# Kernel tuning notes

Measured on AMD Instinct MI355X. Metric: run time of the kernel, lower is better.

The kernel has to match this reference:

```python
import jax, jax.numpy as jnp
import numpy as np

# SectorAttention (PARTNER): dim=256, resolution=(4,4096), H_sp=4, W_sp=1, H=4, heads=8
B, Hq, Hres, Wres, C, NH = 4, 4, 4, 4096, 256, 8
H_SP, W_SP = 4, 1
HD = C // NH
SCALE = HD ** -0.5


def _forward(s, x, s_pos, x_pos, Wq, bq, Wk, bk, Wv, bv, Wo, bo,
             pw1, pb1, bn_g, bn_b, bn_m, bn_v, pw2, pb2,
             ln_g, ln_b, mw1, mb1, mw2, mb2):
    Bb, Lq, Cc = s.shape
    W = Wres
    nW = Bb * (W // W_SP)
    # ---- dynamic relative-position bias (per-window small conv net) ----
    xp = x_pos.reshape(Bb, Hq // H_SP, H_SP, W // W_SP, W_SP, 2)
    xp = jnp.transpose(xp, (0, 1, 3, 5, 2, 4)).reshape(-1, 2, H_SP * W_SP)   # (nW,2,4)
    sp = jnp.transpose(s_pos, (0, 2, 3, 1)).reshape(-1, 2, Hq * W_SP)        # (nW,2,4)
    rel = sp[:, :, :, None] - xp[:, :, None, :]                              # (nW,2,4,4)
    rel = rel.reshape(nW, 2, -1)                                             # (nW,2,16)
    h = jnp.einsum('oc,bcl->bol', pw1, rel) + pb1[None, :, None]             # Conv1d k=1
    h = (h - bn_m[None, :, None]) * jax.lax.rsqrt(bn_v[None, :, None] + 1e-5) \
        * bn_g[None, :, None] + bn_b[None, :, None]                          # BatchNorm1d (eval)
    h = jax.nn.relu(h)
    h = jnp.einsum('oc,bcl->bol', pw2, h) + pb2[None, :, None]               # Conv1d k=1 -> heads
    rel_bias = h.reshape(-1, NH, Hq, H_SP)                                   # (nW,NH,4,4) since W_SP==1
    # ---- projections + window partitioning ----
    q = s @ Wq.T + bq
    q = q.reshape(Bb, Cc, Hq, W)                          # faithful torch .view reinterpretation
    q = q.reshape(Bb, NH, HD, Hq, W // W_SP, W_SP)
    q = jnp.transpose(q, (0, 4, 1, 3, 5, 2)).reshape(-1, NH, Hq * W_SP, HD)

    def im2cswin(t):
        t = jnp.transpose(t, (0, 2, 1)).reshape(Bb, Cc, Hres, W)
        t = t.reshape(Bb, Cc, Hres // H_SP, H_SP, W // W_SP, W_SP)
        t = jnp.transpose(t, (0, 2, 4, 3, 5, 1)).reshape(-1, H_SP * W_SP, Cc)
        return jnp.transpose(t.reshape(-1, H_SP * W_SP, NH, HD), (0, 2, 1, 3))

    k = im2cswin(x @ Wk.T + bk)
    v = im2cswin(x @ Wv.T + bv)
    # ---- windowed attention with dynamic bias ----
    attn = jnp.einsum('wnqd,wnkd->wnqk', q * SCALE, k) + rel_bias
    attn = jax.nn.softmax(attn, axis=-1)
    o = jnp.einsum('wnqk,wnkd->wnqd', attn, v)            # (nW,NH,4,HD)
    o = jnp.transpose(o, (0, 2, 1, 3)).reshape(-1, Hq * W_SP, Cc)
    # windows2img(o, H_sp=Hq, W_sp=W_SP, H=Hq, W=W)
    o = o.reshape(Bb, Hq // Hq, W // W_SP, Hq, W_SP, Cc)
    o = jnp.transpose(o, (0, 1, 3, 2, 4, 5)).reshape(Bb, Hq * W, Cc)
    o = o @ Wo.T + bo
    s1 = s + o
    # ---- LayerNorm + MLP (residual) ----
    mu = jnp.mean(s1, axis=-1, keepdims=True)
    var = jnp.mean((s1 - mu) ** 2, axis=-1, keepdims=True)
    n = (s1 - mu) * jax.lax.rsqrt(var + 1e-5) * ln_g + ln_b
    h2 = jax.nn.gelu(n @ mw1.T + mb1, approximate=False)
    return s1 + h2 @ mw2.T + mb2


def setup_inputs() -> dict:
    key = jax.random.key(0)
    ks = jax.random.split(key, 12)
    rn = lambda k, sh, sc=1.0: jax.random.normal(k, sh, dtype=jnp.float32) * sc
    H4 = 4 * C
    return {
        's': rn(ks[0], (B, Hq * Wres, C)),
        'x': rn(ks[1], (B, Hres * Wres, C)),
        's_pos': rn(ks[2], (B, 2, Wres // W_SP, Hq * W_SP)),
        'x_pos': rn(ks[3], (B, Hres * Wres, 2)),
        'Wq': rn(ks[4], (C, C), 0.02), 'bq': jnp.zeros((C,), jnp.float32),
        'Wk': rn(ks[5], (C, C), 0.02), 'bk': jnp.zeros((C,), jnp.float32),
        'Wv': rn(ks[6], (C, C), 0.02), 'bv': jnp.zeros((C,), jnp.float32),
        'Wo': rn(ks[7], (C, C), 0.02), 'bo': jnp.zeros((C,), jnp.float32),
        'pw1': rn(ks[8], (16, 2), 0.2), 'pb1': jnp.zeros((16,), jnp.float32),
        'bn_g': jnp.ones((16,), jnp.float32), 'bn_b': jnp.zeros((16,), jnp.float32),
        'bn_m': jnp.zeros((16,), jnp.float32), 'bn_v': jnp.ones((16,), jnp.float32),
        'pw2': rn(ks[9], (NH, 16), 0.2), 'pb2': jnp.zeros((NH,), jnp.float32),
        'ln_g': jnp.ones((C,), jnp.float32), 'ln_b': jnp.zeros((C,), jnp.float32),
        'mw1': rn(ks[10], (H4, C), 0.02), 'mb1': jnp.zeros((H4,), jnp.float32),
        'mw2': rn(ks[11], (C, H4), 0.02), 'mb2': jnp.zeros((C,), jnp.float32),
    }


def reference(s, x, s_pos, x_pos, Wq, bq, Wk, bk, Wv, bv, Wo, bo,
              pw1, pb1, bn_g, bn_b, bn_m, bn_v, pw2, pb2,
              ln_g, ln_b, mw1, mb1, mw2, mb2):
    return _forward(s, x, s_pos, x_pos, Wq, bq, Wk, bk, Wv, bv, Wo, bo,
                    pw1, pb1, bn_g, bn_b, bn_m, bn_v, pw2, pb2,
                    ln_g, ln_b, mw1, mb1, mw2, mb2)
```

## Files before the change

### kernel.cpp

```cpp
#include <hip/hip_runtime.h>
#include <hip/hip_bf16.h>
#include <math.h>

typedef __hip_bfloat16 BF;
typedef __bf16 bf16x8 __attribute__((ext_vector_type(8)));
typedef float f32x4 __attribute__((ext_vector_type(4)));

struct alignas(8) BF4 { BF v[4]; };

static __device__ __forceinline__ float b2f(BF x) { return __bfloat162float(x); }
static __device__ __forceinline__ BF f2b(float x) { return __float2bfloat16(x); }

static __device__ __forceinline__ void gld_lds16(const void* g, void* l) {
  __builtin_amdgcn_global_load_lds(
      (const __attribute__((address_space(1))) unsigned int*)g,
      (__attribute__((address_space(3))) unsigned int*)l, 16, 0, 0);
}

__global__ void __launch_bounds__(256) cvt_kernel(
    const float* __restrict__ in, BF* __restrict__ out, int n4) {
  for (int i = blockIdx.x * 256 + threadIdx.x; i < n4; i += gridDim.x * 256) {
    float4 v = ((const float4*)in)[i];
    BF4 o;
    o.v[0] = f2b(v.x); o.v[1] = f2b(v.y); o.v[2] = f2b(v.z); o.v[3] = f2b(v.w);
    ((BF4*)out)[i] = o;
  }
}

__global__ void __launch_bounds__(256) cvt_kv_kernel(
    const float* __restrict__ Wk, const float* __restrict__ Wv,
    const float* __restrict__ bk, const float* __restrict__ bv,
    BF* __restrict__ Wkv, float* __restrict__ bkv) {
  int u = blockIdx.x * 256 + threadIdx.x;
  int r = u >> 5, c8 = u & 31;
  const float* src = ((r & 1) ? Wv : Wk) + (size_t)(r >> 1) * 256 + c8 * 8;
  float4 a = ((const float4*)src)[0];
  float4 b = ((const float4*)src)[1];
  BF tmp[8];
  tmp[0] = f2b(a.x); tmp[1] = f2b(a.y); tmp[2] = f2b(a.z); tmp[3] = f2b(a.w);
  tmp[4] = f2b(b.x); tmp[5] = f2b(b.y); tmp[6] = f2b(b.z); tmp[7] = f2b(b.w);
  *(bf16x8*)(Wkv + (size_t)r * 256 + c8 * 8) = *(bf16x8*)tmp;
  if (u < 512) bkv[u] = ((u & 1) ? bv : bk)[u >> 1];
}

__global__ void __launch_bounds__(256) bias_kernel(
    const float* __restrict__ s_pos, const float* __restrict__ x_pos,
    const float* __restrict__ pw1, const float* __restrict__ pb1,
    const float* __restrict__ bn_g, const float* __restrict__ bn_b,
    const float* __restrict__ bn_m, const float* __restrict__ bn_v,
    const float* __restrict__ pw2, const float* __restrict__ pb2,
    float* __restrict__ out) {
  int gid = blockIdx.x * 256 + threadIdx.x;
  int w = gid >> 4, l = gid & 15;
  int b = w >> 12, wi = w & 4095;
  int i = l >> 2, j = l & 3;
  int e0 = i, e1 = 4 + i;
  float sp0 = s_pos[(((size_t)b * 2 + (e0 & 1)) * 4096 + wi) * 4 + (e0 >> 1)];
  float sp1 = s_pos[(((size_t)b * 2 + (e1 & 1)) * 4096 + wi) * 4 + (e1 >> 1)];
  float xp0 = x_pos[((size_t)b * 16384 + j * 4096 + wi) * 2 + 0];
  float xp1 = x_pos[((size_t)b * 16384 + j * 4096 + wi) * 2 + 1];
  float r0 = sp0 - xp0, r1 = sp1 - xp1;
  float acc[8];
#pragma unroll
  for (int p = 0; p < 8; ++p) acc[p] = pb2[p];
#pragma unroll
  for (int o = 0; o < 16; ++o) {
    float t = pw1[o * 2 + 0] * r0 + pw1[o * 2 + 1] * r1 + pb1[o];
    float sc = bn_g[o] / sqrtf(bn_v[o] + 1e-5f);
    t = (t - bn_m[o]) * sc + bn_b[o];
    t = fmaxf(t, 0.0f);
#pragma unroll
    for (int p = 0; p < 8; ++p) acc[p] += pw2[p * 16 + o] * t;
  }
#pragma unroll
  for (int p = 0; p < 8; ++p) out[(size_t)w * 128 + p * 16 + l] = acc[p];
}

enum { EPI_NONE = 0, EPI_RES = 1, EPI_GELU = 2 };

template <int EPI, typename AT, typename RT, typename CT>
__global__ void __launch_bounds__(256, 2) gemm_tn(
    const AT* __restrict__ A, const BF* __restrict__ Bw,
    const float* __restrict__ bias, const RT* __restrict__ Res,
    CT* __restrict__ C, int M, int N, int K) {
  constexpr bool F32A = __is_same(AT, float);
  alignas(16) __shared__ BF As[2][8][128][8];
  alignas(16) __shared__ BF Bs[2][8][128][8];
  const int ntiles = N >> 7;
  const int cpx = gridDim.x >> 3;
  const int bid = blockIdx.x;
  const int swz = (bid & 7) * cpx + (bid >> 3);
  const int mt = swz / ntiles, nt = swz % ntiles;
  const int row0 = mt << 7, col0 = nt << 7;
  const int t = threadIdx.x;
  const int wave = t >> 6, lane = t & 63;
  const int wr = wave >> 1, wc = wave & 1;
  const int sm = t & 127;
  const int skc = t >> 7;
  f32x4 acc[4][4] = {};
  const int NT = K >> 6;
  float4 ar[4][2];

  auto stageB = [&](int kt, int dbuf) {
#pragma unroll
    for (int i = 0; i < 4; ++i) {
      const int kc = i * 2 + skc;
      gld_lds16(Bw + (size_t)(col0 + sm) * K + kt * 64 + kc * 8,
                &Bs[dbuf][0][0][0] + (size_t)(i * 256 + wave * 64) * 8);
    }
  };
  auto loadA = [&](int kt) {
    if constexpr (F32A) {
#pragma unroll
      for (int i = 0; i < 4; ++i) {
        const int kc = i * 2 + skc;
        const float* src = A + (size_t)(row0 + sm) * K + kt * 64 + kc * 8;
        ar[i][0] = ((const float4*)src)[0];
        ar[i][1] = ((const float4*)src)[1];
      }
    }
  };
  auto writeA = [&](int dbuf) {
    if constexpr (F32A) {
#pragma unroll
      for (int i = 0; i < 4; ++i) {
        const int kc = i * 2 + skc;
        BF tmp[8];
        tmp[0] = f2b(ar[i][0].x); tmp[1] = f2b(ar[i][0].y);
        tmp[2] = f2b(ar[i][0].z); tmp[3] = f2b(ar[i][0].w);
        tmp[4] = f2b(ar[i][1].x); tmp[5] = f2b(ar[i][1].y);
        tmp[6] = f2b(ar[i][1].z); tmp[7] = f2b(ar[i][1].w);
        *(bf16x8*)(&As[dbuf][kc][sm][0]) = *(bf16x8*)tmp;
      }
    }
  };
  auto stageA_bf = [&](int kt, int dbuf) {
    if constexpr (!F32A) {
#pragma unroll
      for (int i = 0; i < 4; ++i) {
        const int kc = i * 2 + skc;
        gld_lds16((const BF*)A + (size_t)(row0 + sm) * K + kt * 64 + kc * 8,
                  &As[dbuf][0][0][0] + (size_t)(i * 256 + wave * 64) * 8);
      }
    }
  };
  auto compute = [&](int dbuf) {
#pragma unroll
    for (int kk = 0; kk < 2; ++kk) {
      const int chunk = kk * 4 + (lane >> 4);
      const int rl = lane & 15;
      bf16x8 af[4], bfr[4];
#pragma unroll
      for (int mi = 0; mi < 4; ++mi)
        af[mi] = *(const bf16x8*)(&As[dbuf][chunk][wr * 64 + mi * 16 + rl][0]);
#pragma unroll
      for (int ni = 0; ni < 4; ++ni)
        bfr[ni] = *(const bf16x8*)(&Bs[dbuf][chunk][wc * 64 + ni * 16 + rl][0]);
#pragma unroll
      for (int mi = 0; mi < 4; ++mi)
#pragma unroll
        for (int ni = 0; ni < 4; ++ni)
          acc[mi][ni] = __builtin_amdgcn_mfma_f32_16x16x32_bf16(
              af[mi], bfr[ni], acc[mi][ni], 0, 0, 0);
    }
  };

  loadA(0); stageA_bf(0, 0); stageB(0, 0); writeA(0);
  __syncthreads();
  int cur = 0;
  for (int kt = 0; kt < NT; ++kt) {
    const bool more = (kt + 1 < NT);
    if (more) {
      loadA(kt + 1);
      stageA_bf(kt + 1, cur ^ 1);
      stageB(kt + 1, cur ^ 1);
    }
    compute(cur);
    if (more) writeA(cur ^ 1);
    __syncthreads();
    cur ^= 1;
  }

  const int rl = lane & 15, rg = lane >> 4;
#pragma unroll
  for (int mi = 0; mi < 4; ++mi) {
#pragma unroll
    for (int ni = 0; ni < 4; ++ni) {
      const int col = col0 + wc * 64 + ni * 16 + rl;
      const float bcol = bias[col];
#pragma unroll
      for (int r = 0; r < 4; ++r) {
        const int row = row0 + wr * 64 + mi * 16 + rg * 4 + r;
        float v = acc[mi][ni][r] + bcol;
        if constexpr (EPI == EPI_GELU)
          v = 0.5f * v * (1.0f + erff(v * 0.70710678118654752f));
        if constexpr (EPI == EPI_RES) {
          if constexpr (__is_same(RT, float))
            v += Res[(size_t)row * N + col];
          else
            v += b2f(Res[(size_t)row * N + col]);
        }
        if constexpr (__is_same(CT, float))
          C[(size_t)row * N + col] = v;
        else
          C[(size_t)row * N + col] = f2b(v);
      }
    }
  }
}

__global__ void __launch_bounds__(256) attn_kernel(
    const BF* __restrict__ Q, const BF* __restrict__ KV,
    const float* __restrict__ bias, BF* __restrict__ O) {
  const int bid = blockIdx.x;
  const int cq = bid & 3, p = (bid >> 2) & 3, hi = (bid >> 4) & 15, b = bid >> 8;
  const int t = threadIdx.x;
  const float SCALE = 0.17677669529663689f;
  __shared__ BF Qlds[256][64];

  {
    const int rloc = t >> 3, cg = t & 7;
#pragma unroll
    for (int it = 0; it < 8; ++it) {
      const int r = it * 32 + rloc;
      const int h = r >> 7, qi = (r >> 5) & 3, hd = r & 31;
      const int nh = p * 2 + h;
      const int l = nh * 2048 + hd * 64 + qi * 16 + hi;
      bf16x8 v = *(const bf16x8*)(Q + ((size_t)b * 16384 + l) * 256 + cq * 64 + cg * 8);
      *(bf16x8*)(&Qlds[r][(cg ^ (r & 7)) * 8]) = v;
    }
  }
  __syncthreads();

  const int g = t >> 5, hd = t & 31;
  const int wbase = hi * 256 + cq * 64;
  for (int c8 = 0; c8 < 8; ++c8) {
    const int c = g * 8 + c8;
    const int wi = wbase + c;
    const int w = b * 4096 + wi;
    const float bias_l = bias[(size_t)w * 128 + (p * 2 + (hd >> 4)) * 16 + (hd & 15)];
#pragma unroll
    for (int h = 0; h < 2; ++h) {
      const int nh = p * 2 + h;
      float qv[4];
#pragma unroll
      for (int qi = 0; qi < 4; ++qi) {
        const int r = h * 128 + qi * 32 + hd;
        qv[qi] = b2f(Qlds[r][(((c >> 3) ^ (hd & 7)) << 3) | (c & 7)]) * SCALE;
      }
      float kf[4], vf[4];
#pragma unroll
      for (int kj = 0; kj < 4; ++kj) {
        const unsigned int kvp = *(const unsigned int*)(
            KV + ((size_t)(b * 16384 + kj * 4096 + wi)) * 512 + ((nh * 32 + hd) << 1));
        kf[kj] = __uint_as_float(kvp << 16);
        vf[kj] = __uint_as_float(kvp & 0xffff0000u);
      }
      float sc[16];
#pragma unroll
      for (int qi = 0; qi < 4; ++qi)
#pragma unroll
        for (int kj = 0; kj < 4; ++kj) {
          float pp = qv[qi] * kf[kj];
          pp += __shfl_xor(pp, 1);
          pp += __shfl_xor(pp, 2);
          pp += __shfl_xor(pp, 4);
          pp += __shfl_xor(pp, 8);
          pp += __shfl_xor(pp, 16);
          sc[qi * 4 + kj] = pp;
        }
#pragma unroll
      for (int idx = 0; idx < 16; ++idx)
        sc[idx] += __shfl(bias_l, (t & 32) + h * 16 + idx);
#pragma unroll
      for (int qi = 0; qi < 4; ++qi) {
        float s0 = sc[qi * 4], s1 = sc[qi * 4 + 1], s2 = sc[qi * 4 + 2], s3 = sc[qi * 4 + 3];
        float mx = fmaxf(fmaxf(s0, s1), fmaxf(s2, s3));
        float e0 = __expf(s0 - mx), e1 = __expf(s1 - mx);
        float e2 = __expf(s2 - mx), e3 = __expf(s3 - mx);
        float inv = 1.0f / (e0 + e1 + e2 + e3);
        float o = (e0 * vf[0] + e1 * vf[1] + e2 * vf[2] + e3 * vf[3]) * inv;
        O[((size_t)b * 16384 + qi * 4096 + wi) * 256 + nh * 32 + hd] = f2b(o);
      }
    }
  }
}

__global__ void __launch_bounds__(256) ln_kernel(
    const BF* __restrict__ S1, const float* __restrict__ g,
    const float* __restrict__ be, BF* __restrict__ Nout) {
  const int wave = threadIdx.x >> 6, lane = threadIdx.x & 63;
  const size_t row = (size_t)blockIdx.x * 4 + wave;
  BF4 d = *(const BF4*)(S1 + row * 256 + lane * 4);
  float x[4] = {b2f(d.v[0]), b2f(d.v[1]), b2f(d.v[2]), b2f(d.v[3])};
  float s = x[0] + x[1] + x[2] + x[3];
  float sq = x[0] * x[0] + x[1] * x[1] + x[2] * x[2] + x[3] * x[3];
#pragma unroll
  for (int m = 1; m <= 32; m <<= 1) {
    s += __shfl_xor(s, m);
    sq += __shfl_xor(sq, m);
  }
  const float mean = s * 0.00390625f;
  const float var = sq * 0.00390625f - mean * mean;
  const float rstd = 1.0f / sqrtf(var + 1e-5f);
  BF4 o;
#pragma unroll
  for (int jj = 0; jj < 4; ++jj) {
    float nv = (x[jj] - mean) * rstd * g[lane * 4 + jj] + be[lane * 4 + jj];
    o.v[jj] = f2b(nv);
  }
  *(BF4*)(Nout + row * 256 + lane * 4) = o;
}

extern "C" void kernel_launch(void* const* d_in, const int* in_sizes, int n_in,
                              void* d_out, int out_size, void* d_ws, size_t ws_size,
                              hipStream_t stream) {
  const float* s     = (const float*)d_in[0];
  const float* x     = (const float*)d_in[1];
  const float* s_pos = (const float*)d_in[2];
  const float* x_pos = (const float*)d_in[3];
  const float* Wq = (const float*)d_in[4];  const float* bq = (const float*)d_in[5];
  const float* Wk = (const float*)d_in[6];  const float* bk = (const float*)d_in[7];
  const float* Wv = (const float*)d_in[8];  const float* bv = (const float*)d_in[9];
  const float* Wo = (const float*)d_in[10]; const float* bo = (const float*)d_in[11];
  const float* pw1 = (const float*)d_in[12]; const float* pb1 = (const float*)d_in[13];
  const float* bn_g = (const float*)d_in[14]; const float* bn_b = (const float*)d_in[15];
  const float* bn_m = (const float*)d_in[16]; const float* bn_v = (const float*)d_in[17];
  const float* pw2 = (const float*)d_in[18]; const float* pb2 = (const float*)d_in[19];
  const float* ln_g = (const float*)d_in[20]; const float* ln_b = (const float*)d_in[21];
  const float* mw1 = (const float*)d_in[22]; const float* mb1 = (const float*)d_in[23];
  const float* mw2 = (const float*)d_in[24]; const float* mb2 = (const float*)d_in[25];

  char* ws = (char*)d_ws;
  float* biasb = (float*)ws;
  BF* Qw   = (BF*)(ws + 8388608);
  BF* KVw  = (BF*)(ws + 41943040);
  BF* S1   = (BF*)(ws + 109051904);
  BF* Wq_bf  = (BF*)(ws + 142606336);
  BF* Wo_bf  = (BF*)(ws + 142737408);
  BF* Wkv_bf = (BF*)(ws + 142868480);
  BF* mw1_bf = (BF*)(ws + 143130624);
  BF* mw2_bf = (BF*)(ws + 143654912);
  float* bkv = (float*)(ws + 144179200);
  BF* Nw = Qw;
  BF* H2 = KVw;
  BF* ObBF = (BF*)d_out;
  float* Of = (float*)d_out;

  cvt_kernel<<<64, 256, 0, stream>>>(Wq, Wq_bf, 16384);
  cvt_kernel<<<64, 256, 0, stream>>>(Wo, Wo_bf, 16384);
  cvt_kernel<<<256, 256, 0, stream>>>(mw1, mw1_bf, 65536);
  cvt_kernel<<<256, 256, 0, stream>>>(mw2, mw2_bf, 65536);
  cvt_kv_kernel<<<64, 256, 0, stream>>>(Wk, Wv, bk, bv, Wkv_bf, bkv);
  bias_kernel<<<1024, 256, 0, stream>>>(s_pos, x_pos, pw1, pb1, bn_g, bn_b,
                                        bn_m, bn_v, pw2, pb2, biasb);

  gemm_tn<EPI_NONE, float, float, BF><<<1024, 256, 0, stream>>>(
      s, Wq_bf, bq, nullptr, Qw, 65536, 256, 256);
  gemm_tn<EPI_NONE, float, float, BF><<<2048, 256, 0, stream>>>(
      x, Wkv_bf, bkv, nullptr, KVw, 65536, 512, 256);
  attn_kernel<<<1024, 256, 0, stream>>>(Qw, KVw, biasb, ObBF);
  gemm_tn<EPI_RES, BF, float, BF><<<1024, 256, 0, stream>>>(
      ObBF, Wo_bf, bo, s, S1, 65536, 256, 256);
  ln_kernel<<<16384, 256, 0, stream>>>(S1, ln_g, ln_b, Nw);
  for (int h = 0; h < 2; ++h) {
    const size_t ro = (size_t)h * 32768;
    gemm_tn<EPI_GELU, BF, float, BF><<<2048, 256, 0, stream>>>(
        Nw + ro * 256, mw1_bf, mb1, nullptr, H2, 32768, 1024, 256);
    gemm_tn<EPI_RES, BF, BF, float><<<512, 256, 0, stream>>>(
        H2, mw2_bf, mb2, S1 + ro * 256, Of + ro * 256, 32768, 256, 1024);
  }
}
```

Baseline: 458.2 us.

## Fuse Q scaling and window layout into Q GEMM, restructure attention per window

Adds a dedicated Q projection GEMM that applies bias and softmax scale and writes Q directly in a per-window, per-head contiguous layout. The attention kernel then reads Q and K with wide vector loads instead of staging a gathered Q tile in LDS and doing shuffle-reduction dot products. It computes one score per lane with 16 lanes per head-window, uses a small shuffle softmax, and writes 8 outputs per lane. The K/V weights become non-interleaved (K block then V block), so KV rows are [K|V] rather than interleaved pairs. This relies on the generic GEMM output layout matching the new indexing.

```diff
diff --git a/kernel.cpp b/kernel.cpp
--- a/kernel.cpp
+++ b/kernel.cpp
@@ -7,6 +7,7 @@
 typedef float f32x4 __attribute__((ext_vector_type(4)));
 
 struct alignas(8) BF4 { BF v[4]; };
+struct alignas(16) BF8 { BF v[8]; };
 
 static __device__ __forceinline__ float b2f(BF x) { return __bfloat162float(x); }
 static __device__ __forceinline__ BF f2b(float x) { return __float2bfloat16(x); }
@@ -27,20 +28,11 @@
   }
 }
 
-__global__ void __launch_bounds__(256) cvt_kv_kernel(
-    const float* __restrict__ Wk, const float* __restrict__ Wv,
+__global__ void __launch_bounds__(256) bkv_kernel(
     const float* __restrict__ bk, const float* __restrict__ bv,
-    BF* __restrict__ Wkv, float* __restrict__ bkv) {
-  int u = blockIdx.x * 256 + threadIdx.x;
-  int r = u >> 5, c8 = u & 31;
-  const float* src = ((r & 1) ? Wv : Wk) + (size_t)(r >> 1) * 256 + c8 * 8;
-  float4 a = ((const float4*)src)[0];
-  float4 b = ((const float4*)src)[1];
-  BF tmp[8];
-  tmp[0] = f2b(a.x); tmp[1] = f2b(a.y); tmp[2] = f2b(a.z); tmp[3] = f2b(a.w);
-  tmp[4] = f2b(b.x); tmp[5] = f2b(b.y); tmp[6] = f2b(b.z); tmp[7] = f2b(b.w);
-  *(bf16x8*)(Wkv + (size_t)r * 256 + c8 * 8) = *(bf16x8*)tmp;
-  if (u < 512) bkv[u] = ((u & 1) ? bv : bk)[u >> 1];
+    float* __restrict__ bkv) {
+  int i = blockIdx.x * 256 + threadIdx.x;
+  bkv[i] = (i < 256) ? bk[i] : bv[i - 256];
 }
 
 __global__ void __launch_bounds__(256) bias_kernel(
@@ -209,81 +201,174 @@
   }
 }
 
+__global__ void __launch_bounds__(256, 2) gemm_q(
+    const float* __restrict__ A, const BF* __restrict__ Bw,
+    const float* __restrict__ bias, BF* __restrict__ Qa) {
+  constexpr int K = 256;
+  alignas(16) __shared__ BF As[2][8][128][8];
+  alignas(16) __shared__ BF Bs[2][8][128][8];
+  const int cpx = gridDim.x >> 3;
+  const int bid = blockIdx.x;
+  const int swz = (bid & 7) * cpx + (bid >> 3);
+  const int mt = swz >> 1, nt = swz & 1;
+  const int hp = mt & 3, qi = (mt >> 2) & 3, nh = (mt >> 4) & 7, bb = mt >> 7;
+  const int col0 = nt << 7;
+  const int t = threadIdx.x;
+  const int wave = t >> 6, lane = t & 63;
+  const int wr = wave >> 1, wc = wave & 1;
+  const int sm = t & 127;
+  const int skc = t >> 7;
+  const size_t grow = (size_t)bb * 16384 + nh * 2048 + (size_t)(sm & 31) * 64 +
+                      qi * 16 + hp * 4 + (sm >> 5);
+  f32x4 acc[4][4] = {};
+  float4 ar[4][2];
+
+  auto stageB = [&](int kt, int dbuf) {
+#pragma unroll
+    for (int i = 0; i < 4; ++i) {
+      const int kc = i * 2 + skc;
+      gld_lds16(Bw + (size_t)(col0 + sm) * K + kt * 64 + kc * 8,
+                &Bs[dbuf][0][0][0] + (size_t)(i * 256 + wave * 64) * 8);
+    }
+  };
+  auto loadA = [&](int kt) {
+#pragma unroll
+    for (int i = 0; i < 4; ++i) {
+      const int kc = i * 2 + skc;
+      const float* src = A + grow * K + kt * 64 + kc * 8;
+      ar[i][0] = ((const float4*)src)[0];
+      ar[i][1] = ((const float4*)src)[1];
+    }
+  };
+  auto writeA = [&](int dbuf) {
+#pragma unroll
+    for (int i = 0; i < 4; ++i) {
+      const int kc = i * 2 + skc;
+      BF tmp[8];
+      tmp[0] = f2b(ar[i][0].x); tmp[1] = f2b(ar[i][0].y);
+      tmp[2] = f2b(ar[i][0].z); tmp[3] = f2b(ar[i][0].w);
+      tmp[4] = f2b(ar[i][1].x); tmp[5] = f2b(ar[i][1].y);
+      tmp[6] = f2b(ar[i][1].z); tmp[7] = f2b(ar[i][1].w);
+      *(bf16x8*)(&As[dbuf][kc][sm][0]) = *(bf16x8*)tmp;
+    }
+  };
+  auto compute = [&](int dbuf) {
+#pragma unroll
+    for (int kk = 0; kk < 2; ++kk) {
+      const int chunk = kk * 4 + (lane >> 4);
+      const int rl = lane & 15;
+      bf16x8 af[4], bfr[4];
+#pragma unroll
+      for (int mi = 0; mi < 4; ++mi)
+        af[mi] = *(const bf16x8*)(&As[dbuf][chunk][wr * 64 + mi * 16 + rl][0]);
+#pragma unroll
+      for (int ni = 0; ni < 4; ++ni)
+        bfr[ni] = *(const bf16x8*)(&Bs[dbuf][chunk][wc * 64 + ni * 16 + rl][0]);
+#pragma unroll
+      for (int mi = 0; mi < 4; ++mi)
+#pragma unroll
+        for (int ni = 0; ni < 4; ++ni)
+          acc[mi][ni] = __builtin_amdgcn_mfma_f32_16x16x32_bf16(
+              af[mi], bfr[ni], acc[mi][ni], 0, 0, 0);
+    }
+  };
+
+  loadA(0); stageB(0, 0); writeA(0);
+  __syncthreads();
+  int cur = 0;
+  for (int kt = 0; kt < 4; ++kt) {
+    const bool more = (kt + 1 < 4);
+    if (more) { loadA(kt + 1); stageB(kt + 1, cur ^ 1); }
+    compute(cur);
+    if (more) writeA(cur ^ 1);
+    __syncthreads();
+    cur ^= 1;
+  }
+
+  const int rl = lane & 15, rg = lane >> 4;
+  const float SCALE = 0.17677669529663689f;
+#pragma unroll
+  for (int mi = 0; mi < 4; ++mi) {
+#pragma unroll
+    for (int ni = 0; ni < 4; ++ni) {
+      const int col = col0 + wc * 64 + ni * 16 + rl;
+      const float bcol = bias[col];
+      const int i0 = wr * 64 + mi * 16 + rg * 4;
+      const int hd = i0 & 31, hil = i0 >> 5;
+      const int wi = (hp * 4 + hil) * 256 + col;
+      BF4 pk;
+#pragma unroll
+      for (int r = 0; r < 4; ++r)
+        pk.v[r] = f2b((acc[mi][ni][r] + bcol) * SCALE);
+      *(BF4*)(Qa + ((((size_t)bb * 4096 + wi) * 8 + nh) * 128 + qi * 32 + hd)) = pk;
+    }
+  }
+}
+
 __global__ void __launch_bounds__(256) attn_kernel(
-    const BF* __restrict__ Q, const BF* __restrict__ KV,
-    const float* __restrict__ bias, BF* __restrict__ O) {
-  const int bid = blockIdx.x;
-  const int cq = bid & 3, p = (bid >> 2) & 3, hi = (bid >> 4) & 15, b = bid >> 8;
+    const BF* __restrict__ Qa, const BF* __restrict__ KV,
+    const float* __restrict__ biasb, BF* __restrict__ O) {
   const int t = threadIdx.x;
-  const float SCALE = 0.17677669529663689f;
-  __shared__ BF Qlds[256][64];
-
-  {
-    const int rloc = t >> 3, cg = t & 7;
-#pragma unroll
-    for (int it = 0; it < 8; ++it) {
-      const int r = it * 32 + rloc;
-      const int h = r >> 7, qi = (r >> 5) & 3, hd = r & 31;
-      const int nh = p * 2 + h;
-      const int l = nh * 2048 + hd * 64 + qi * 16 + hi;
-      bf16x8 v = *(const bf16x8*)(Q + ((size_t)b * 16384 + l) * 256 + cq * 64 + cg * 8);
-      *(bf16x8*)(&Qlds[r][(cg ^ (r & 7)) * 8]) = v;
-    }
-  }
-  __syncthreads();
-
-  const int g = t >> 5, hd = t & 31;
-  const int wbase = hi * 256 + cq * 64;
-  for (int c8 = 0; c8 < 8; ++c8) {
-    const int c = g * 8 + c8;
-    const int wi = wbase + c;
-    const int w = b * 4096 + wi;
-    const float bias_l = bias[(size_t)w * 128 + (p * 2 + (hd >> 4)) * 16 + (hd & 15)];
-#pragma unroll
-    for (int h = 0; h < 2; ++h) {
-      const int nh = p * 2 + h;
-      float qv[4];
-#pragma unroll
-      for (int qi = 0; qi < 4; ++qi) {
-        const int r = h * 128 + qi * 32 + hd;
-        qv[qi] = b2f(Qlds[r][(((c >> 3) ^ (hd & 7)) << 3) | (c & 7)]) * SCALE;
-      }
-      float kf[4], vf[4];
-#pragma unroll
-      for (int kj = 0; kj < 4; ++kj) {
-        const unsigned int kvp = *(const unsigned int*)(
-            KV + ((size_t)(b * 16384 + kj * 4096 + wi)) * 512 + ((nh * 32 + hd) << 1));
-        kf[kj] = __uint_as_float(kvp << 16);
-        vf[kj] = __uint_as_float(kvp & 0xffff0000u);
-      }
-      float sc[16];
-#pragma unroll
-      for (int qi = 0; qi < 4; ++qi)
-#pragma unroll
-        for (int kj = 0; kj < 4; ++kj) {
-          float pp = qv[qi] * kf[kj];
-          pp += __shfl_xor(pp, 1);
-          pp += __shfl_xor(pp, 2);
-          pp += __shfl_xor(pp, 4);
-          pp += __shfl_xor(pp, 8);
-          pp += __shfl_xor(pp, 16);
-          sc[qi * 4 + kj] = pp;
-        }
-#pragma unroll
-      for (int idx = 0; idx < 16; ++idx)
-        sc[idx] += __shfl(bias_l, (t & 32) + h * 16 + idx);
-#pragma unroll
-      for (int qi = 0; qi < 4; ++qi) {
-        float s0 = sc[qi * 4], s1 = sc[qi * 4 + 1], s2 = sc[qi * 4 + 2], s3 = sc[qi * 4 + 3];
-        float mx = fmaxf(fmaxf(s0, s1), fmaxf(s2, s3));
-        float e0 = __expf(s0 - mx), e1 = __expf(s1 - mx);
-        float e2 = __expf(s2 - mx), e3 = __expf(s3 - mx);
-        float inv = 1.0f / (e0 + e1 + e2 + e3);
-        float o = (e0 * vf[0] + e1 * vf[1] + e2 * vf[2] + e3 * vf[3]) * inv;
-        O[((size_t)b * 16384 + qi * 4096 + wi) * 256 + nh * 32 + hd] = f2b(o);
-      }
-    }
-  }
+  const int g = t >> 4, l16 = t & 15;
+  const int qi = l16 >> 2, kj = l16 & 3;
+  const int w = (blockIdx.x << 1) | (g >> 3);
+  const int nh = g & 7;
+  const int b = w >> 12, wi = w & 4095;
+
+  const uint4* qp = (const uint4*)(Qa + ((((size_t)b * 4096 + wi) * 8 + nh) * 128 + qi * 32));
+  uint4 qv[4] = {qp[0], qp[1], qp[2], qp[3]};
+  const uint4* kp = (const uint4*)(KV + ((size_t)b * 16384 + kj * 4096 + wi) * 512 + nh * 32);
+  uint4 kv[4] = {kp[0], kp[1], kp[2], kp[3]};
+  const float bias_l = biasb[(size_t)w * 128 + nh * 16 + l16];
+  const BF* vbase = KV + (size_t)b * 16384 * 512 + 256 + nh * 32 + kj * 8;
+  uint4 vv[4];
+#pragma unroll
+  for (int d = 0; d < 4; ++d)
+    vv[d] = *(const uint4*)(vbase + ((size_t)((kj ^ d) * 4096 + wi)) * 512);
+
+  float accs[4] = {0.f, 0.f, 0.f, 0.f};
+#pragma unroll
+  for (int j = 0; j < 4; ++j) {
+#pragma unroll
+    for (int e = 0; e < 4; ++e) {
+      unsigned qe = ((const unsigned*)&qv[j])[e];
+      unsigned ke = ((const unsigned*)&kv[j])[e];
+      float ql = __uint_as_float(qe << 16);
+      float qh = __uint_as_float(qe & 0xffff0000u);
+      float kl = __uint_as_float(ke << 16);
+      float kh = __uint_as_float(ke & 0xffff0000u);
+      accs[e] = fmaf(ql, kl, accs[e]);
+      accs[e] = fmaf(qh, kh, accs[e]);
+    }
+  }
+  const float score = accs[0] + accs[1] + accs[2] + accs[3] + bias_l;
+
+  float mx = fmaxf(score, __shfl_xor(score, 1));
+  mx = fmaxf(mx, __shfl_xor(mx, 2));
+  float e = __expf(score - mx);
+  float sm = e + __shfl_xor(e, 1);
+  sm += __shfl_xor(sm, 2);
+  float p = e / sm;
+  float pd[4];
+  pd[0] = p;
+  pd[1] = __shfl_xor(p, 1);
+  pd[2] = __shfl_xor(p, 2);
+  pd[3] = __shfl_xor(pd[1], 2);
+
+  float o8[8] = {0.f, 0.f, 0.f, 0.f, 0.f, 0.f, 0.f, 0.f};
+#pragma unroll
+  for (int d = 0; d < 4; ++d) {
+#pragma unroll
+    for (int e = 0; e < 4; ++e) {
+      unsigned ve = ((const unsigned*)&vv[d])[e];
+      o8[e * 2 + 0] = fmaf(pd[d], __uint_as_float(ve << 16), o8[e * 2 + 0]);
+      o8[e * 2 + 1] = fmaf(pd[d], __uint_as_float(ve & 0xffff0000u), o8[e * 2 + 1]);
+    }
+  }
+  BF8 ob;
+#pragma unroll
+  for (int h = 0; h < 8; ++h) ob.v[h] = f2b(o8[h]);
+  *(BF8*)(O + ((size_t)b * 16384 + qi * 4096 + wi) * 256 + nh * 32 + kj * 8) = ob;
 }
 
 __global__ void __launch_bounds__(256) ln_kernel(
@@ -333,7 +418,7 @@
 
   char* ws = (char*)d_ws;
   float* biasb = (float*)ws;
-  BF* Qw   = (BF*)(ws + 8388608);
+  BF* Qa   = (BF*)(ws + 8388608);
   BF* KVw  = (BF*)(ws + 41943040);
   BF* S1   = (BF*)(ws + 109051904);
   BF* Wq_bf  = (BF*)(ws + 142606336);
@@ -342,24 +427,25 @@
   BF* mw1_bf = (BF*)(ws + 143130624);
   BF* mw2_bf = (BF*)(ws + 143654912);
   float* bkv = (float*)(ws + 144179200);
-  BF* Nw = Qw;
+  BF* Nw = Qa;
   BF* H2 = KVw;
   BF* ObBF = (BF*)d_out;
   float* Of = (float*)d_out;
 
   cvt_kernel<<<64, 256, 0, stream>>>(Wq, Wq_bf, 16384);
   cvt_kernel<<<64, 256, 0, stream>>>(Wo, Wo_bf, 16384);
+  cvt_kernel<<<64, 256, 0, stream>>>(Wk, Wkv_bf, 16384);
+  cvt_kernel<<<64, 256, 0, stream>>>(Wv, Wkv_bf + 65536, 16384);
   cvt_kernel<<<256, 256, 0, stream>>>(mw1, mw1_bf, 65536);
   cvt_kernel<<<256, 256, 0, stream>>>(mw2, mw2_bf, 65536);
-  cvt_kv_kernel<<<64, 256, 0, stream>>>(Wk, Wv, bk, bv, Wkv_bf, bkv);
+  bkv_kernel<<<2, 256, 0, stream>>>(bk, bv, bkv);
   bias_kernel<<<1024, 256, 0, stream>>>(s_pos, x_pos, pw1, pb1, bn_g, bn_b,
                                         bn_m, bn_v, pw2, pb2, biasb);
 
-  gemm_tn<EPI_NONE, float, float, BF><<<1024, 256, 0, stream>>>(
-      s, Wq_bf, bq, nullptr, Qw, 65536, 256, 256);
+  gemm_q<<<1024, 256, 0, stream>>>(s, Wq_bf, bq, Qa);
   gemm_tn<EPI_NONE, float, float, BF><<<2048, 256, 0, stream>>>(
       x, Wkv_bf, bkv, nullptr, KVw, 65536, 512, 256);
-  attn_kernel<<<1024, 256, 0, stream>>>(Qw, KVw, biasb, ObBF);
+  attn_kernel<<<8192, 256, 0, stream>>>(Qa, KVw, biasb, ObBF);
   gemm_tn<EPI_RES, BF, float, BF><<<1024, 256, 0, stream>>>(
       ObBF, Wo_bf, bo, s, S1, 65536, 256, 256);
   ln_kernel<<<16384, 256, 0, stream>>>(S1, ln_g, ln_b, Nw);
```

After: 419.9 us. 1.09x faster.
